# Optimization experiments

Hardware: AMD Instinct MI355X
Metric: run time of the kernel (lower is better)

Reference implementation:

```python
import jax, jax.numpy as jnp
import numpy as np


def _lsa(cost):
    """Exact rectangular linear sum assignment (Jonker-Volgenant / e-maxx
    Hungarian with potentials). Returns (row_ind, col_ind) matching
    scipy.optimize.linear_sum_assignment (row_ind sorted ascending)."""
    n, m = cost.shape
    transposed = n > m
    if transposed:
        cost = cost.T
        n, m = m, n
    cost = np.asarray(cost, dtype=np.float64)
    INF = 1e18
    u = np.zeros(n + 1)
    v = np.zeros(m + 1)
    p = np.zeros(m + 1, dtype=np.int64)   # p[j]: 1-based row assigned to col j
    way = np.zeros(m + 1, dtype=np.int64)
    for i in range(1, n + 1):
        p[0] = i
        j0 = 0
        minv = np.full(m + 1, INF)
        used = np.zeros(m + 1, dtype=bool)
        while True:
            used[j0] = True
            i0 = p[j0]
            cur = cost[i0 - 1] - u[i0] - v[1:]          # vectorized over cols
            upd = (~used[1:]) & (cur < minv[1:])
            minv[1:] = np.where(upd, cur, minv[1:])
            way[1:] = np.where(upd, j0, way[1:])
            masked = np.where(used[1:], INF, minv[1:])
            j1 = int(np.argmin(masked)) + 1
            delta = masked[j1 - 1]
            u[p[used]] += delta
            v[used] -= delta
            minv[1:] = np.where(used[1:], minv[1:], minv[1:] - delta)
            j0 = j1
            if p[j0] == 0:
                break
        while j0 != 0:
            j1 = way[j0]
            p[j0] = p[j1]
            j0 = j1
    if transposed:
        pairs = sorted((j - 1, p[j] - 1) for j in range(1, m + 1) if p[j] != 0)
    else:
        pairs = sorted((p[j] - 1, j - 1) for j in range(1, m + 1) if p[j] != 0)
    row_ind = np.array([r for r, _ in pairs], dtype=np.int64)
    col_ind = np.array([c for _, c in pairs], dtype=np.int64)
    return row_ind, col_ind


def _row_order(cost_b):
    """Matched rows first (scipy order), then unmatched rows sorted ascending."""
    N = cost_b.shape[0]
    row_ind, _ = _lsa(cost_b)
    remain = sorted(set(range(N)) - set(row_ind.tolist()))
    return np.concatenate([row_ind, np.asarray(remain, dtype=np.int64)])


def _pairwise_l2(seq1, seq2):
    # Fused batched cdist: ||a-b|| = sqrt(|a|^2 + |b|^2 - 2 a.b)
    a2 = jnp.sum(seq1 * seq1, axis=-1)[:, :, None]   # [B,N,1]
    b2 = jnp.sum(seq2 * seq2, axis=-1)[:, None, :]   # [B,1,M]
    ab = jnp.einsum('bnd,bmd->bnm', seq1, seq2)      # [B,N,M]
    return jnp.sqrt(jnp.maximum(a2 + b2 - 2.0 * ab, 0.0))


def setup_inputs() -> dict:
    key = jax.random.key(0)
    k1, k2 = jax.random.split(key)
    B, N, M, D = 16, 512, 448, 1536
    return {
        'seq1': jax.random.normal(k1, (B, N, D), dtype=jnp.float32),
        'seq2': jax.random.normal(k2, (B, M, D), dtype=jnp.float32),
    }


def reference(seq1, seq2):
    cost = np.asarray(_pairwise_l2(seq1, seq2))      # [B,N,M], one fused kernel
    # Hungarian solve is inherently sequential / CPU-bound per batch element.
    perm = np.stack([_row_order(cost[b]) for b in range(cost.shape[0])], 0)
    perm = jnp.asarray(perm)                         # [B,N]
    return jnp.take_along_axis(seq1, perm[:, :, None], axis=1)
```

## Files before the change

kernel.cpp:

```cpp
#include <hip/hip_runtime.h>
#include <math.h>

#define BB 16
#define NN 512
#define MM 448
#define DD 1536

constexpr int TK = 32;

__global__ __launch_bounds__(256) void cost_kernel(const float* __restrict__ s1,
                                                   const float* __restrict__ s2,
                                                   float* __restrict__ Ct) {
  __shared__ float As[TK][68];
  __shared__ float Bs[TK][68];
  const int b = blockIdx.z;
  const int ibase = blockIdx.x * 64;
  const int jbase = blockIdx.y * 64;
  const int tid = threadIdx.x;
  const float* s1b = s1 + ((size_t)b * NN + ibase) * DD;
  const float* s2b = s2 + ((size_t)b * MM + jbase) * DD;
  const int ix = (tid & 15) * 4;
  const int jy = (tid >> 4) * 4;
  double acc[16];
#pragma unroll
  for (int t = 0; t < 16; ++t) acc[t] = 0.0;

  for (int k0 = 0; k0 < DD; k0 += TK) {
#pragma unroll
    for (int rep = 0; rep < 2; ++rep) {
      int idx = tid + rep * 256;
      int r = idx >> 3;
      int c4 = (idx & 7) * 4;
      float4 a = *(const float4*)(s1b + (size_t)r * DD + k0 + c4);
      As[c4 + 0][r] = a.x; As[c4 + 1][r] = a.y; As[c4 + 2][r] = a.z; As[c4 + 3][r] = a.w;
      float4 bb = *(const float4*)(s2b + (size_t)r * DD + k0 + c4);
      Bs[c4 + 0][r] = bb.x; Bs[c4 + 1][r] = bb.y; Bs[c4 + 2][r] = bb.z; Bs[c4 + 3][r] = bb.w;
    }
    __syncthreads();
    float pacc[16];
#pragma unroll
    for (int t = 0; t < 16; ++t) pacc[t] = 0.f;
#pragma unroll 8
    for (int kk = 0; kk < TK; ++kk) {
      float4 av = *(const float4*)&As[kk][ix];
      float4 bv = *(const float4*)&Bs[kk][jy];
      float a[4] = {av.x, av.y, av.z, av.w};
      float bq[4] = {bv.x, bv.y, bv.z, bv.w};
#pragma unroll
      for (int t = 0; t < 4; ++t)
#pragma unroll
        for (int q = 0; q < 4; ++q) {
          float d = a[t] - bq[q];
          pacc[t * 4 + q] = fmaf(d, d, pacc[t * 4 + q]);
        }
    }
#pragma unroll
    for (int t = 0; t < 16; ++t) acc[t] += (double)pacc[t];
    __syncthreads();
  }
#pragma unroll
  for (int t = 0; t < 4; ++t)
#pragma unroll
    for (int q = 0; q < 4; ++q) {
      int i = ibase + ix + t;
      int jj = jbase + jy + q;
      float d2 = (float)acc[t * 4 + q];
      Ct[((size_t)b * MM + jj) * NN + i] = sqrtf(fmaxf(d2, 0.f));
    }
}

__device__ __forceinline__ unsigned wave_min_bcast_u32(unsigned x) {
  int v = (int)x;
#define ST(C) { int o = __builtin_amdgcn_update_dpp(-1, v, C, 0xF, 0xF, false); \
                v = ((unsigned)o < (unsigned)v) ? o : v; }
  ST(0x111) ST(0x112) ST(0x114) ST(0x118) ST(0x142) ST(0x143)
#undef ST
  return (unsigned)__builtin_amdgcn_readlane(v, 63);
}

__device__ __forceinline__ double wave_min_bcast_f64_fast(double x) {
  union DU { double d; unsigned u[2]; };
  DU v; v.d = x;
  unsigned hmin = wave_min_bcast_u32(v.u[1]);
  unsigned lc = (v.u[1] == hmin) ? v.u[0] : 0xFFFFFFFFu;
  unsigned lmin = wave_min_bcast_u32(lc);
  DU r; r.u[0] = lmin; r.u[1] = hmin;
  return r.d;
}

__device__ __forceinline__ float wave_min_bcast_f32(float x) {
  union FU { float f; int i; };
  FU v; v.f = x;
  const int INFB = 0x7f7fffff;
#define DPP1(CTRL) { FU o; \
  o.i = __builtin_amdgcn_update_dpp(INFB, v.i, CTRL, 0xF, 0xF, false); \
  if (o.f < v.f) v.f = o.f; }
  DPP1(0x111) DPP1(0x112) DPP1(0x114) DPP1(0x118) DPP1(0x142) DPP1(0x143)
#undef DPP1
  FU r; r.i = __builtin_amdgcn_readlane(v.i, 63);
  return r.f;
}

__global__ __launch_bounds__(64) void jv_kernel(const float* __restrict__ Ct,
                                                int* __restrict__ perm) {
  const int b = blockIdx.x;
  const float* C = Ct + (size_t)b * MM * NN;
  __shared__ double u_lds[MM + 1];
  __shared__ int p_lds[NN + 1];
  __shared__ int way_lds[NN + 1];
  __shared__ int colOwner[NN];
  __shared__ int rowMatched[MM];
  __shared__ int freeL[MM];
  __shared__ int nfree_s;
  __shared__ int cnt_lds[64];
  const int lane = threadIdx.x;
  const int jbase = 8 * lane + 1;

  if (lane == 0) u_lds[0] = 0.0;
  for (int t = lane; t <= NN; t += 64) { p_lds[t] = 0; way_lds[t] = 0; }
  for (int t = lane; t < NN; t += 64) colOwner[t] = -1;
  for (int t = lane; t < MM; t += 64) rowMatched[t] = 0;
  asm volatile("s_waitcnt lgkmcnt(0)" ::: "memory");

  for (int r = 0; r < MM; ++r) {
    const float4* r4 = (const float4*)(C + (size_t)r * NN);
    float4 ca = r4[2 * lane];
    float4 cb = r4[2 * lane + 1];
    float c[8] = {ca.x, ca.y, ca.z, ca.w, cb.x, cb.y, cb.z, cb.w};
    float lm = 1e30f; int la = 0;
#pragma unroll
    for (int q = 0; q < 8; ++q)
      if (c[q] < lm) { lm = c[q]; la = 8 * lane + q; }
    float rm = wave_min_bcast_f32(lm);
    unsigned long long bm = __ballot(lm == rm);
    int sl = (int)__ffsll((unsigned long long)bm) - 1;
    int jc = __builtin_amdgcn_readlane(la, sl);
    if (lane == 0) {
      u_lds[r + 1] = (double)rm;
      if (colOwner[jc] < 0) {
        colOwner[jc] = r;
        rowMatched[r] = 1;
        p_lds[jc + 1] = r + 1;
      }
    }
  }
  double vcol[8];
#pragma unroll
  for (int q = 0; q < 8; ++q) vcol[q] = 0.0;
  asm volatile("s_waitcnt lgkmcnt(0)" ::: "memory");

  if (lane == 0) {
    int n = 0;
    for (int r = 0; r < MM; ++r) if (!rowMatched[r]) freeL[n++] = r;
    nfree_s = n;
  }
  asm volatile("s_waitcnt lgkmcnt(0)" ::: "memory");
  int nfree = nfree_s;

  for (int pass = 0; pass < 2; ++pass) {
    int prev = nfree; nfree = 0; int k = 0;
    while (k < prev) {
      const int i = freeL[k]; k++;
      const float4* r4 = (const float4*)(C + (size_t)i * NN);
      float4 ca = r4[2 * lane];
      float4 cb = r4[2 * lane + 1];
      float c[8] = {ca.x, ca.y, ca.z, ca.w, cb.x, cb.y, cb.z, cb.w};
      double m1 = 1e18, m2 = 1e18; int a1 = 0;
#pragma unroll
      for (int q = 0; q < 8; ++q) {
        double h = (double)c[q] - vcol[q];
        if (h < m1) { m2 = m1; m1 = h; a1 = 8 * lane + q; }
        else if (h < m2) m2 = h;
      }
      double umin = wave_min_bcast_f64_fast(m1);
      unsigned long long bm = __ballot(m1 == umin);
      int sl = (int)__ffsll((unsigned long long)bm) - 1;
      int j1 = __builtin_amdgcn_readlane(a1, sl);
      double cd = (lane == sl) ? m2 : m1;
      double usub = wave_min_bcast_f64_fast(cd);
      const bool strict = (umin < usub);
      if (strict && (j1 >> 3) == lane) {
        double dec = usub - umin;
#pragma unroll
        for (int qq = 0; qq < 8; ++qq) if (qq == (j1 & 7)) vcol[qq] -= dec;
      }
      const int powner = p_lds[j1 + 1];
      asm volatile("" ::: "memory");
      const int i0 = powner - 1;
      if (lane == 0) { u_lds[i + 1] = usub; p_lds[j1 + 1] = i + 1; }
      if (i0 >= 0) {
        if (strict) { k--; if (lane == 0) freeL[k] = i0; }
        else        { if (lane == 0) freeL[nfree] = i0; nfree++; }
      }
      asm volatile("s_waitcnt lgkmcnt(0)" ::: "memory");
    }
  }

  const int nf3 = nfree;
  for (int fi = 0; fi < nf3; ++fi) {
    const int i = freeL[fi] + 1;
    if (lane == 0) p_lds[0] = i;
    double minv[8], rec[8];
    int preg[8];
#pragma unroll
    for (int q = 0; q < 8; ++q) { minv[q] = 1e18; rec[q] = 0.0; preg[q] = 0; }
    int usedm = 0;
    double cum = 0.0;
    int j0 = 0, i0 = i;
    asm volatile("s_waitcnt lgkmcnt(0)" ::: "memory");

    while (true) {
#pragma unroll
      for (int q = 0; q < 8; ++q)
        if (j0 == jbase + q) {
          usedm |= (1 << q); preg[q] = i0; rec[q] = cum; minv[q] = 1e18;
        }

      const float4* r4 = (const float4*)(C + (size_t)(i0 - 1) * NN);
      float4 ca = r4[2 * lane];
      float4 cb = r4[2 * lane + 1];
      double uu = u_lds[i0];
      float c[8] = {ca.x, ca.y, ca.z, ca.w, cb.x, cb.y, cb.z, cb.w};
#pragma unroll
      for (int q = 0; q < 8; ++q) {
        if (!((usedm >> q) & 1)) {
          double cur = ((double)c[q] - uu) - vcol[q];
          cur = (cur > 0.0) ? cur : 0.0;
          if (cur < minv[q]) { minv[q] = cur; way_lds[jbase + q] = j0; }
        }
      }
      double m01 = (minv[1] < minv[0]) ? minv[1] : minv[0];
      int    a01 = (minv[1] < minv[0]) ? jbase + 1 : jbase + 0;
      double m23 = (minv[3] < minv[2]) ? minv[3] : minv[2];
      int    a23 = (minv[3] < minv[2]) ? jbase + 3 : jbase + 2;
      double m45 = (minv[5] < minv[4]) ? minv[5] : minv[4];
      int    a45 = (minv[5] < minv[4]) ? jbase + 5 : jbase + 4;
      double m67 = (minv[7] < minv[6]) ? minv[7] : minv[6];
      int    a67 = (minv[7] < minv[6]) ? jbase + 7 : jbase + 6;
      double m03 = (m23 < m01) ? m23 : m01;
      int    a03 = (m23 < m01) ? a23 : a01;
      double m47 = (m67 < m45) ? m67 : m45;
      int    a47 = (m67 < m45) ? a67 : a45;
      double lm = (m47 < m03) ? m47 : m03;
      int    la = (m47 < m03) ? a47 : a03;

      int pcand = p_lds[la];

      union DU { double d; unsigned u[2]; };
      DU lv; lv.d = lm;
      unsigned hmin = wave_min_bcast_u32(lv.u[1]);
      unsigned lc = (lv.u[1] == hmin) ? lv.u[0] : 0xFFFFFFFFu;
      unsigned lmin = wave_min_bcast_u32(lc);
      unsigned long long bm = __ballot((lv.u[1] == hmin) && (lv.u[0] == lmin));
      int sl = (int)__ffsll((unsigned long long)bm) - 1;
      int j1 = __builtin_amdgcn_readlane(la, sl);
      int pn = __builtin_amdgcn_readlane(pcand, sl);
      DU dd; dd.u[0] = lmin; dd.u[1] = hmin;
      double delta = dd.d;
      cum += delta;
#pragma unroll
      for (int q = 0; q < 8; ++q) minv[q] -= delta;
      j0 = j1;
      if (pn == 0) break;
      i0 = pn;
    }

    if (lane == 0) u_lds[i] += cum;
#pragma unroll
    for (int q = 0; q < 8; ++q)
      if ((usedm >> q) & 1) {
        double d = cum - rec[q];
        vcol[q] -= d;
        u_lds[preg[q]] += d;
      }
    asm volatile("s_waitcnt lgkmcnt(0)" ::: "memory");
    if (lane == 0) {
      int jj = j0;
      while (jj != 0) { int jp = way_lds[jj]; p_lds[jj] = p_lds[jp]; jj = jp; }
    }
    asm volatile("s_waitcnt lgkmcnt(0)" ::: "memory");
  }

  int mask = 0, cnt = 0;
#pragma unroll
  for (int q = 0; q < 8; ++q)
    if (p_lds[jbase + q] != 0) { mask |= 1 << q; cnt++; }
  cnt_lds[lane] = cnt;
  asm volatile("s_waitcnt lgkmcnt(0)" ::: "memory");
  int pre = 0;
  for (int l = 0; l < 64; ++l) { int cl = cnt_lds[l]; if (l < lane) pre += cl; }
  int mpos = pre;
  int upos = MM + (8 * lane - pre);
#pragma unroll
  for (int q = 0; q < 8; ++q) {
    int col = 8 * lane + q;
    if ((mask >> q) & 1) perm[b * NN + mpos++] = col;
    else                 perm[b * NN + upos++] = col;
  }
}

__global__ __launch_bounds__(256) void gather_kernel(const float* __restrict__ s1,
                                                     const int* __restrict__ perm,
                                                     float* __restrict__ out) {
  const int bi = blockIdx.x;
  const int b = bi >> 9;
  const int src = perm[bi];
  const float4* sp = (const float4*)(s1 + ((size_t)b * NN + src) * DD);
  float4* dp = (float4*)(out + (size_t)bi * DD);
  for (int t = threadIdx.x; t < DD / 4; t += 256) dp[t] = sp[t];
}

extern "C" void kernel_launch(void* const* d_in, const int* in_sizes, int n_in,
                              void* d_out, int out_size, void* d_ws, size_t ws_size,
                              hipStream_t stream) {
  const float* s1 = (const float*)d_in[0];
  const float* s2 = (const float*)d_in[1];
  float* out = (float*)d_out;
  float* Ct = (float*)d_out;
  int* perm = (int*)d_ws;

  dim3 cg(NN / 64, MM / 64, BB);
  cost_kernel<<<cg, 256, 0, stream>>>(s1, s2, Ct);
  jv_kernel<<<BB, 64, 0, stream>>>(Ct, perm);
  gather_kernel<<<BB * NN, 256, 0, stream>>>(s1, perm, out);
}
```

Before: 6.797 ms.

## Prefetch cost rows ahead in Hungarian phases and keep way array in registers

```diff
diff --git a/kernel.cpp b/kernel.cpp
--- a/kernel.cpp
+++ b/kernel.cpp
@@ -122,26 +122,33 @@
   for (int t = lane; t < MM; t += 64) rowMatched[t] = 0;
   asm volatile("s_waitcnt lgkmcnt(0)" ::: "memory");
 
-  for (int r = 0; r < MM; ++r) {
-    const float4* r4 = (const float4*)(C + (size_t)r * NN);
-    float4 ca = r4[2 * lane];
-    float4 cb = r4[2 * lane + 1];
-    float c[8] = {ca.x, ca.y, ca.z, ca.w, cb.x, cb.y, cb.z, cb.w};
-    float lm = 1e30f; int la = 0;
-#pragma unroll
-    for (int q = 0; q < 8; ++q)
-      if (c[q] < lm) { lm = c[q]; la = 8 * lane + q; }
-    float rm = wave_min_bcast_f32(lm);
-    unsigned long long bm = __ballot(lm == rm);
-    int sl = (int)__ffsll((unsigned long long)bm) - 1;
-    int jc = __builtin_amdgcn_readlane(la, sl);
-    if (lane == 0) {
-      u_lds[r + 1] = (double)rm;
-      if (colOwner[jc] < 0) {
-        colOwner[jc] = r;
-        rowMatched[r] = 1;
-        p_lds[jc + 1] = r + 1;
-      }
+  {
+    const float4* r40 = (const float4*)(C);
+    const float4* r41 = (const float4*)(C + (size_t)NN);
+    float4 ca = r40[2 * lane], cb = r40[2 * lane + 1];
+    float4 na = r41[2 * lane], nb = r41[2 * lane + 1];
+    for (int r = 0; r < MM; ++r) {
+      int rp = (r + 2 < MM) ? (r + 2) : (MM - 1);
+      const float4* r4n = (const float4*)(C + (size_t)rp * NN);
+      float4 pa = r4n[2 * lane], pb = r4n[2 * lane + 1];
+      float c[8] = {ca.x, ca.y, ca.z, ca.w, cb.x, cb.y, cb.z, cb.w};
+      float lm = 1e30f; int la = 0;
+#pragma unroll
+      for (int q = 0; q < 8; ++q)
+        if (c[q] < lm) { lm = c[q]; la = 8 * lane + q; }
+      float rm = wave_min_bcast_f32(lm);
+      unsigned long long bm = __ballot(lm == rm);
+      int sl = (int)__ffsll((unsigned long long)bm) - 1;
+      int jc = __builtin_amdgcn_readlane(la, sl);
+      if (lane == 0) {
+        u_lds[r + 1] = (double)rm;
+        if (colOwner[jc] < 0) {
+          colOwner[jc] = r;
+          rowMatched[r] = 1;
+          p_lds[jc + 1] = r + 1;
+        }
+      }
+      ca = na; cb = nb; na = pa; nb = pb;
     }
   }
   double vcol[8];
@@ -159,40 +166,60 @@
 
   for (int pass = 0; pass < 2; ++pass) {
     int prev = nfree; nfree = 0; int k = 0;
-    while (k < prev) {
-      const int i = freeL[k]; k++;
-      const float4* r4 = (const float4*)(C + (size_t)i * NN);
-      float4 ca = r4[2 * lane];
-      float4 cb = r4[2 * lane + 1];
-      float c[8] = {ca.x, ca.y, ca.z, ca.w, cb.x, cb.y, cb.z, cb.w};
-      double m1 = 1e18, m2 = 1e18; int a1 = 0;
-#pragma unroll
-      for (int q = 0; q < 8; ++q) {
-        double h = (double)c[q] - vcol[q];
-        if (h < m1) { m2 = m1; m1 = h; a1 = 8 * lane + q; }
-        else if (h < m2) m2 = h;
-      }
-      double umin = wave_min_bcast_f64_fast(m1);
-      unsigned long long bm = __ballot(m1 == umin);
-      int sl = (int)__ffsll((unsigned long long)bm) - 1;
-      int j1 = __builtin_amdgcn_readlane(a1, sl);
-      double cd = (lane == sl) ? m2 : m1;
-      double usub = wave_min_bcast_f64_fast(cd);
-      const bool strict = (umin < usub);
-      if (strict && (j1 >> 3) == lane) {
-        double dec = usub - umin;
-#pragma unroll
-        for (int qq = 0; qq < 8; ++qq) if (qq == (j1 & 7)) vcol[qq] -= dec;
-      }
-      const int powner = p_lds[j1 + 1];
-      asm volatile("" ::: "memory");
-      const int i0 = powner - 1;
-      if (lane == 0) { u_lds[i + 1] = usub; p_lds[j1 + 1] = i + 1; }
-      if (i0 >= 0) {
-        if (strict) { k--; if (lane == 0) freeL[k] = i0; }
-        else        { if (lane == 0) freeL[nfree] = i0; nfree++; }
-      }
-      asm volatile("s_waitcnt lgkmcnt(0)" ::: "memory");
+    if (prev == 0) continue;
+    int i = freeL[0];
+    {
+      const float4* r4p = (const float4*)(C + (size_t)i * NN);
+      float4 ca = r4p[2 * lane];
+      float4 cb = r4p[2 * lane + 1];
+      while (true) {
+        const int kn = k + 1;
+        const int ig = (kn < prev) ? freeL[kn] : 0;
+        const float4* r4n = (const float4*)(C + (size_t)ig * NN);
+        float4 nca = r4n[2 * lane];
+        float4 ncb = r4n[2 * lane + 1];
+
+        float c[8] = {ca.x, ca.y, ca.z, ca.w, cb.x, cb.y, cb.z, cb.w};
+        double m1 = 1e18, m2 = 1e18; int a1 = 0;
+#pragma unroll
+        for (int q = 0; q < 8; ++q) {
+          double h = (double)c[q] - vcol[q];
+          if (h < m1) { m2 = m1; m1 = h; a1 = 8 * lane + q; }
+          else if (h < m2) m2 = h;
+        }
+        double umin = wave_min_bcast_f64_fast(m1);
+        unsigned long long bm = __ballot(m1 == umin);
+        int sl = (int)__ffsll((unsigned long long)bm) - 1;
+        int j1 = __builtin_amdgcn_readlane(a1, sl);
+        double cd = (lane == sl) ? m2 : m1;
+        double usub = wave_min_bcast_f64_fast(cd);
+        const bool strict = (umin < usub);
+        if (strict && (j1 >> 3) == lane) {
+          double dec = usub - umin;
+#pragma unroll
+          for (int qq = 0; qq < 8; ++qq) if (qq == (j1 & 7)) vcol[qq] -= dec;
+        }
+        const int powner = p_lds[j1 + 1];
+        asm volatile("" ::: "memory");
+        const int i0 = powner - 1;
+        if (lane == 0) { u_lds[i + 1] = usub; p_lds[j1 + 1] = i + 1; }
+        const bool reproc = (i0 >= 0) && strict;
+        if (i0 >= 0 && !strict) {
+          if (lane == 0) freeL[nfree] = i0;
+          nfree++;
+        }
+        asm volatile("s_waitcnt lgkmcnt(0)" ::: "memory");
+        if (reproc) {
+          i = i0;
+          const float4* r4m = (const float4*)(C + (size_t)i * NN);
+          ca = r4m[2 * lane];
+          cb = r4m[2 * lane + 1];
+        } else {
+          k = kn;
+          if (k >= prev) break;
+          i = ig; ca = nca; cb = ncb;
+        }
+      }
     }
   }
 
@@ -201,32 +228,27 @@
     const int i = freeL[fi] + 1;
     if (lane == 0) p_lds[0] = i;
     double minv[8], rec[8];
-    int preg[8];
-#pragma unroll
-    for (int q = 0; q < 8; ++q) { minv[q] = 1e18; rec[q] = 0.0; preg[q] = 0; }
+    int preg[8], wayr[8];
+#pragma unroll
+    for (int q = 0; q < 8; ++q) { minv[q] = 1e18; rec[q] = 0.0; preg[q] = 0; wayr[q] = 0; }
     int usedm = 0;
     double cum = 0.0;
     int j0 = 0, i0 = i;
     asm volatile("s_waitcnt lgkmcnt(0)" ::: "memory");
 
+    const float4* r4p = (const float4*)(C + (size_t)(i0 - 1) * NN);
+    float4 ca = r4p[2 * lane];
+    float4 cb = r4p[2 * lane + 1];
+    double uu = u_lds[i0];
+
     while (true) {
-#pragma unroll
-      for (int q = 0; q < 8; ++q)
-        if (j0 == jbase + q) {
-          usedm |= (1 << q); preg[q] = i0; rec[q] = cum; minv[q] = 1e18;
-        }
-
-      const float4* r4 = (const float4*)(C + (size_t)(i0 - 1) * NN);
-      float4 ca = r4[2 * lane];
-      float4 cb = r4[2 * lane + 1];
-      double uu = u_lds[i0];
       float c[8] = {ca.x, ca.y, ca.z, ca.w, cb.x, cb.y, cb.z, cb.w};
 #pragma unroll
       for (int q = 0; q < 8; ++q) {
         if (!((usedm >> q) & 1)) {
           double cur = ((double)c[q] - uu) - vcol[q];
           cur = (cur > 0.0) ? cur : 0.0;
-          if (cur < minv[q]) { minv[q] = cur; way_lds[jbase + q] = j0; }
+          if (cur < minv[q]) { minv[q] = cur; wayr[q] = j0; }
         }
       }
       double m01 = (minv[1] < minv[0]) ? minv[1] : minv[0];
@@ -246,6 +268,17 @@
 
       int pcand = p_lds[la];
 
+      float lmf = (float)lm;
+      float rmf = wave_min_bcast_f32(lmf);
+      unsigned long long bmf = __ballot(lmf == rmf);
+      int slf = (int)__ffsll(bmf) - 1;
+      int pnf = __builtin_amdgcn_readlane(pcand, slf);
+      int rs = (pnf > 0) ? (pnf - 1) : 0;
+      const float4* r4s = (const float4*)(C + (size_t)rs * NN);
+      float4 sca = r4s[2 * lane];
+      float4 scb = r4s[2 * lane + 1];
+      double uus = u_lds[pnf];
+
       union DU { double d; unsigned u[2]; };
       DU lv; lv.d = lm;
       unsigned hmin = wave_min_bcast_u32(lv.u[1]);
@@ -262,17 +295,32 @@
       for (int q = 0; q < 8; ++q) minv[q] -= delta;
       j0 = j1;
       if (pn == 0) break;
+#pragma unroll
+      for (int q = 0; q < 8; ++q)
+        if (j1 == jbase + q) {
+          usedm |= (1 << q); preg[q] = pn; rec[q] = cum; minv[q] = 1e18;
+        }
       i0 = pn;
+      if (pn == pnf) {
+        ca = sca; cb = scb; uu = uus;
+      } else {
+        const float4* r4m = (const float4*)(C + (size_t)(pn - 1) * NN);
+        ca = r4m[2 * lane];
+        cb = r4m[2 * lane + 1];
+        uu = u_lds[pn];
+      }
     }
 
     if (lane == 0) u_lds[i] += cum;
 #pragma unroll
-    for (int q = 0; q < 8; ++q)
+    for (int q = 0; q < 8; ++q) {
+      way_lds[jbase + q] = wayr[q];
       if ((usedm >> q) & 1) {
         double d = cum - rec[q];
         vcol[q] -= d;
         u_lds[preg[q]] += d;
       }
+    }
     asm volatile("s_waitcnt lgkmcnt(0)" ::: "memory");
     if (lane == 0) {
       int jj = j0;
```

New measurement: 6.409 ms. 5.7% less time.
